# Kernel optimization log

Hardware: AMD Instinct MI355X
Metric: run time of the kernel (lower is better)

Reference implementation:

```python
import jax, jax.numpy as jnp
import numpy as np

N_NODES = 50000
N_EDGES = 1600000
IN_FEATS = 128
ENC_H = 20
DEC_H = 64


def setup_inputs() -> dict:
    key = jax.random.key(0)
    ks = jax.random.split(key, 8)
    x = jax.random.normal(ks[0], (N_NODES, IN_FEATS), dtype=jnp.float32)
    edge_index = jax.random.randint(ks[1], (2, N_EDGES), 0, N_NODES, dtype=jnp.int64)
    eps = jax.random.uniform(ks[2], (N_EDGES, 1), dtype=jnp.float32)
    # GCNConv weight [in, out] and bias
    W_gcn = jax.random.normal(ks[3], (IN_FEATS, ENC_H), dtype=jnp.float32) / np.sqrt(IN_FEATS)
    b_gcn = jnp.zeros((ENC_H,), dtype=jnp.float32)
    # decoder: Linear(60,64) -> ReLU -> Linear(64,1)
    LATENT = 3 * ENC_H
    W1 = jax.random.normal(ks[4], (LATENT, DEC_H), dtype=jnp.float32) / np.sqrt(LATENT)
    b1 = jnp.zeros((DEC_H,), dtype=jnp.float32)
    W2 = jax.random.normal(ks[5], (DEC_H, 1), dtype=jnp.float32) / np.sqrt(DEC_H)
    b2 = jnp.zeros((1,), dtype=jnp.float32)
    return {"x": x, "edge_index": edge_index, "node_id": 123, "eps": eps,
            "W_gcn": W_gcn, "b_gcn": b_gcn, "W1": W1, "b1": b1, "W2": W2, "b2": b2}


def _gcn_conv(x, edge_index, W, b):
    """PyG GCNConv: add self-loops, symmetric norm D^-1/2 (A+I) D^-1/2, x@W + b."""
    N = x.shape[0]
    loop = jnp.arange(N, dtype=edge_index.dtype)
    row = jnp.concatenate([edge_index[0], loop])  # source
    col = jnp.concatenate([edge_index[1], loop])  # target
    deg = jax.ops.segment_sum(jnp.ones_like(col, dtype=x.dtype), col, num_segments=N)
    dinv = jnp.where(deg > 0, jax.lax.rsqrt(deg), 0.0)
    norm = dinv[row] * dinv[col]                 # [E+N]
    h = x @ W                                     # [N, enc_h]
    out = jax.ops.segment_sum(norm[:, None] * h[row], col, num_segments=N)
    return out + b


def reference(x, edge_index, node_id, eps, W_gcn, b_gcn, W1, b1, W2, b2):
    h1 = jax.nn.relu(_gcn_conv(x, edge_index, W_gcn, b_gcn))  # [N, enc_h]
    rows, cols = edge_index[0], edge_index[1]
    E = rows.shape[0]
    node_emb = jnp.broadcast_to(h1[node_id], (E, h1.shape[1]))
    z = jnp.concatenate([h1[rows], h1[cols], node_emb], axis=1)  # [E, 3*enc_h]
    w = jax.nn.relu(z @ W1 + b1) @ W2 + b2                       # [E, 1]
    # gumbel-sigmoid reparameterization (training=True, bias=0.0 -> bias=1e-4)
    bias = 0.0001
    e = (bias - (1.0 - bias)) * eps + (1.0 - bias)
    gate = jnp.log(e) - jnp.log1p(-e) + w  # temperature = 1.0
    return jax.nn.sigmoid(gate)
```

## Files before the change

kernel.cpp:

```cpp
#include <hip/hip_runtime.h>
#include <hip/hip_bf16.h>
#include <math.h>

#define NN 50000
#define NE 1600000
#define FIN 128
#define EH 20
#define DH 64

#define BSTEP 64
#define NBK ((NN + BSTEP - 1) / BSTEP)
#define BCAP 3072
#define CHUNK 8192
#define PERT (CHUNK / 256)


__global__ void k_init(int* bcur, int* off, int* flag, const void* ei) {
    int i = threadIdx.x;
    for (int b = i; b < NBK; b += 1024) bcur[b] = b * BCAP;
    if (i == 0) {
        off[NN] = NE;
        const int* w = (const int*)ei;
        int all0 = 1;
        for (int j = 1; j < 128; j += 2) all0 &= (w[j] == 0);
        *flag = all0;
    }
}

__device__ __forceinline__ int ld_col(const void* ei, int w64, size_t idx) {
    return w64 ? (int)((const long long*)ei)[idx] : ((const int*)ei)[idx];
}

__global__ void k_bin(const void* ei, const int* flag,
                      int* __restrict__ bcur, unsigned* __restrict__ binned) {
    __shared__ int hist[NBK];
    __shared__ int gbase[NBK];
    const int base = blockIdx.x * CHUNK;
    for (int i = threadIdx.x; i < NBK; i += 256) hist[i] = 0;
    __syncthreads();
    const int w64 = *flag;
    int myr[PERT], myc[PERT];
#pragma unroll
    for (int i = 0; i < PERT; ++i) {
        int idx = base + threadIdx.x + i * 256;
        if (idx < NE) {
            myr[i] = ld_col(ei, w64, idx);
            int c = ld_col(ei, w64, (size_t)NE + idx);
            myc[i] = c;
            atomicAdd(&hist[c >> 6], 1);
        } else {
            myc[i] = -1;
        }
    }
    __syncthreads();
    for (int b = threadIdx.x; b < NBK; b += 256) {
        int h = hist[b];
        gbase[b] = h ? atomicAdd(&bcur[b], h) : 0;
        hist[b] = 0;
    }
    __syncthreads();
#pragma unroll
    for (int i = 0; i < PERT; ++i) {
        int c = myc[i];
        if (c >= 0) {
            int bkt = c >> 6;
            int pos = gbase[bkt] + atomicAdd(&hist[bkt], 1);
            binned[pos] = (unsigned)myr[i] | ((unsigned)(c & 63) << 16);
        }
    }
}

__global__ void k_sort(const int* __restrict__ bcur, const unsigned* __restrict__ binned,
                       int* __restrict__ off, int* __restrict__ src) {
    __shared__ int red[256];
    __shared__ int hcnt[BSTEP];
    __shared__ int sc[BSTEP];
    __shared__ int hoff[BSTEP];
    __shared__ int cur[BSTEP];
    const int b = blockIdx.x;
    const int nbase = b * BSTEP;
    int part = 0;
    for (int i = threadIdx.x; i < b; i += 256) part += bcur[i] - i * BCAP;
    red[threadIdx.x] = part;
    __syncthreads();
    for (int d = 128; d > 0; d >>= 1) {
        if (threadIdx.x < d) red[threadIdx.x] += red[threadIdx.x + d];
        __syncthreads();
    }
    const int p0 = red[0];
    const int cnt = bcur[b] - b * BCAP;
    const unsigned* rbase = binned + (size_t)b * BCAP;
    if (threadIdx.x < BSTEP) hcnt[threadIdx.x] = 0;
    __syncthreads();
    for (int i = threadIdx.x; i < cnt; i += 256)
        atomicAdd(&hcnt[rbase[i] >> 16], 1);
    __syncthreads();
    int v = 0;
    if (threadIdx.x < BSTEP) { v = hcnt[threadIdx.x]; sc[threadIdx.x] = v; }
    __syncthreads();
    for (int d = 1; d < BSTEP; d <<= 1) {
        int u = 0;
        if (threadIdx.x < BSTEP && threadIdx.x >= d) u = sc[threadIdx.x - d];
        __syncthreads();
        if (threadIdx.x < BSTEP) sc[threadIdx.x] += u;
        __syncthreads();
    }
    if (threadIdx.x < BSTEP) {
        int o = p0 + sc[threadIdx.x] - v;
        hoff[threadIdx.x] = o;
        cur[threadIdx.x] = 0;
        int n = nbase + threadIdx.x;
        if (n < NN) off[n] = o;
    }
    __syncthreads();
    for (int i = threadIdx.x; i < cnt; i += 256) {
        unsigned rec = rbase[i];
        int cl = rec >> 16;
        int pos = hoff[cl] + atomicAdd(&cur[cl], 1);
        src[pos] = (int)(rec & 0xffffu);
    }
}

__global__ void k_xw(const float* __restrict__ x, const float* __restrict__ W,
                     const int* __restrict__ off, __hip_bfloat16* __restrict__ hs16) {
    int t = blockIdx.x * blockDim.x + threadIdx.x;
    int n = t / EH;
    int k = t - n * EH;
    if (n >= NN) return;
    const float4* xr = (const float4*)(x + (size_t)n * FIN);
    float acc = 0.f;
#pragma unroll
    for (int j4 = 0; j4 < FIN / 4; ++j4) {
        float4 v = xr[j4];
        acc = fmaf(v.x, W[(4 * j4 + 0) * EH + k], acc);
        acc = fmaf(v.y, W[(4 * j4 + 1) * EH + k], acc);
        acc = fmaf(v.z, W[(4 * j4 + 2) * EH + k], acc);
        acc = fmaf(v.w, W[(4 * j4 + 3) * EH + k], acc);
    }
    float dinv = rsqrtf(1.0f + (float)(off[n + 1] - off[n]));
    hs16[n * 32 + k] = __float2bfloat16(dinv * acc);
}

__device__ __forceinline__ float blo(unsigned u) { return __uint_as_float(u << 16); }
__device__ __forceinline__ float bhi(unsigned u) { return __uint_as_float(u & 0xffff0000u); }

__global__ void k_gather(const int* __restrict__ off, const int* __restrict__ src,
                         const __hip_bfloat16* __restrict__ hs16,
                         const float* __restrict__ bg, float* __restrict__ h1) {
    int t = blockIdx.x * blockDim.x + threadIdx.x;
    int n = t / 10;
    int kk = t - n * 10;
    if (n >= NN) return;
    const unsigned* hu = (const unsigned*)hs16;
    unsigned self = hu[n * 16 + kk];
    float acc0 = blo(self), acc1 = bhi(self);
    int e0 = off[n], e1 = off[n + 1];
    int e = e0;
    for (; e + 3 < e1; e += 4) {
        int r0 = src[e];
        int r1 = src[e + 1];
        int r2 = src[e + 2];
        int r3 = src[e + 3];
        unsigned v0 = hu[r0 * 16 + kk];
        unsigned v1 = hu[r1 * 16 + kk];
        unsigned v2 = hu[r2 * 16 + kk];
        unsigned v3 = hu[r3 * 16 + kk];
        acc0 += blo(v0); acc1 += bhi(v0);
        acc0 += blo(v1); acc1 += bhi(v1);
        acc0 += blo(v2); acc1 += bhi(v2);
        acc0 += blo(v3); acc1 += bhi(v3);
    }
    for (; e < e1; ++e) {
        unsigned v = hu[src[e] * 16 + kk];
        acc0 += blo(v); acc1 += bhi(v);
    }
    float dinv = rsqrtf(1.0f + (float)(e1 - e0));
    float2 res;
    res.x = fmaxf(fmaf(dinv, acc0, bg[2 * kk]), 0.f);
    res.y = fmaxf(fmaf(dinv, acc1, bg[2 * kk + 1]), 0.f);
    *(float2*)(h1 + (size_t)n * EH + 2 * kk) = res;
}

__global__ void k_ab(const float* __restrict__ h1, const float* __restrict__ W1,
                     const float* __restrict__ b1, const void* nid_p,
                     __hip_bfloat16* __restrict__ A16, __hip_bfloat16* __restrict__ B16) {
    int t = blockIdx.x * blockDim.x + threadIdx.x;
    int n = t >> 6;
    int j = t & 63;
    if (n >= NN) return;
    int nid = *(const int*)nid_p;
    const float* hr = h1 + (size_t)n * EH;
    const float* hn = h1 + (size_t)nid * EH;
    float a = 0.f, b = b1[j];
#pragma unroll
    for (int k = 0; k < EH; ++k) {
        float hv = hr[k];
        a = fmaf(hv, W1[k * DH + j], a);
        b = fmaf(hv, W1[(EH + k) * DH + j], b);
        b = fmaf(hn[k], W1[(2 * EH + k) * DH + j], b);
    }
    A16[(size_t)n * DH + j] = __float2bfloat16(a);
    B16[(size_t)n * DH + j] = __float2bfloat16(b);
}

__global__ void k_edge(const void* ei, const int* flag,
                       const __hip_bfloat16* __restrict__ A16,
                       const __hip_bfloat16* __restrict__ B16,
                       const float* __restrict__ W2, const float* __restrict__ b2,
                       const float* __restrict__ eps, float* __restrict__ out) {
    long long t = (long long)blockIdx.x * blockDim.x + threadIdx.x;
    int e = (int)(t >> 2);
    if (e >= NE) return;
    int q = (int)(t & 3);
    const int w64 = *flag;
    int r = ld_col(ei, w64, e);
    int c = ld_col(ei, w64, (size_t)NE + e);
    const uint4* arow = (const uint4*)(A16 + (size_t)r * DH) + q * 2;
    const uint4* brow = (const uint4*)(B16 + (size_t)c * DH) + q * 2;
    const float* w = W2 + q * 16;
    float acc = 0.f;
#pragma unroll
    for (int j = 0; j < 2; ++j) {
        uint4 av = arow[j];
        uint4 bv = brow[j];
        acc = fmaf(fmaxf(blo(av.x) + blo(bv.x), 0.f), w[8 * j + 0], acc);
        acc = fmaf(fmaxf(bhi(av.x) + bhi(bv.x), 0.f), w[8 * j + 1], acc);
        acc = fmaf(fmaxf(blo(av.y) + blo(bv.y), 0.f), w[8 * j + 2], acc);
        acc = fmaf(fmaxf(bhi(av.y) + bhi(bv.y), 0.f), w[8 * j + 3], acc);
        acc = fmaf(fmaxf(blo(av.z) + blo(bv.z), 0.f), w[8 * j + 4], acc);
        acc = fmaf(fmaxf(bhi(av.z) + bhi(bv.z), 0.f), w[8 * j + 5], acc);
        acc = fmaf(fmaxf(blo(av.w) + blo(bv.w), 0.f), w[8 * j + 6], acc);
        acc = fmaf(fmaxf(bhi(av.w) + bhi(bv.w), 0.f), w[8 * j + 7], acc);
    }
    acc += __shfl_xor(acc, 1);
    acc += __shfl_xor(acc, 2);
    if (q == 0) {
        float ep = eps[e];
        float ee = fmaf(-0.9998f, ep, 0.9999f);
        float om = fmaf(0.9998f, ep, 0.0001f);
        float gate = 0.69314718f * (__builtin_amdgcn_logf(ee) - __builtin_amdgcn_logf(om))
                   + acc + b2[0];
        float tt = __builtin_amdgcn_exp2f(-1.44269504f * gate);
        out[e] = __builtin_amdgcn_rcpf(1.0f + tt);
    }
}


extern "C" void kernel_launch(void* const* d_in, const int* in_sizes, int n_in,
                              void* d_out, int out_size, void* d_ws, size_t ws_size,
                              hipStream_t stream) {
    const float* x   = (const float*)d_in[0];
    const void*  ei  = d_in[1];
    const void*  nid = d_in[2];
    const float* eps = (const float*)d_in[3];
    const float* Wg  = (const float*)d_in[4];
    const float* bg  = (const float*)d_in[5];
    const float* W1  = (const float*)d_in[6];
    const float* b1  = (const float*)d_in[7];
    const float* W2  = (const float*)d_in[8];
    const float* b2  = (const float*)d_in[9];
    float* out = (float*)d_out;

    float* ws = (float*)d_ws;
    unsigned* binned = (unsigned*)(ws + 0);
    int*  src    = (int*)(ws + 2402560);
    __hip_bfloat16* hs16 = (__hip_bfloat16*)(ws + 4002560);
    float* h1    = ws + 4802560;
    __hip_bfloat16* A16 = (__hip_bfloat16*)(ws + 5802752);
    __hip_bfloat16* B16 = (__hip_bfloat16*)(ws + 7402752);
    int* off     = (int*)(ws + 9002752);
    int* bcur    = (int*)(ws + 9053184);
    int* flag    = (int*)(ws + 9054208);

    dim3 blk(256);
    const int nchunk = (NE + CHUNK - 1) / CHUNK;
    k_init<<<1, 1024, 0, stream>>>(bcur, off, flag, ei);
    k_bin<<<nchunk, blk, 0, stream>>>(ei, flag, bcur, binned);
    k_sort<<<NBK, blk, 0, stream>>>(bcur, binned, off, src);
    k_xw<<<(NN * EH + 255) / 256, blk, 0, stream>>>(x, Wg, off, hs16);
    k_gather<<<(NN * 10 + 255) / 256, blk, 0, stream>>>(off, src, hs16, bg, h1);
    k_ab<<<(NN * 64 + 255) / 256, blk, 0, stream>>>(h1, W1, b1, nid, A16, B16);
    k_edge<<<((size_t)NE * 4 + 255) / 256, blk, 0, stream>>>(ei, flag, A16, B16, W2, b2, eps, out);
}
```

Measured before the change: 174.7 us.

## Process edge MLP in target-bucket order and scatter results back via positions

```diff
diff --git a/kernel.cpp b/kernel.cpp
--- a/kernel.cpp
+++ b/kernel.cpp
@@ -13,6 +13,7 @@
 #define BCAP 3072
 #define CHUNK 8192
 #define PERT (CHUNK / 256)
+#define ESPLIT 4
 
 
 __global__ void k_init(int* bcur, int* off, int* flag, const void* ei) {
@@ -32,7 +33,8 @@
 }
 
 __global__ void k_bin(const void* ei, const int* flag,
-                      int* __restrict__ bcur, unsigned* __restrict__ binned) {
+                      int* __restrict__ bcur, unsigned* __restrict__ binned,
+                      int* __restrict__ pos32) {
     __shared__ int hist[NBK];
     __shared__ int gbase[NBK];
     const int base = blockIdx.x * CHUNK;
@@ -66,6 +68,7 @@
             int bkt = c >> 6;
             int pos = gbase[bkt] + atomicAdd(&hist[bkt], 1);
             binned[pos] = (unsigned)myr[i] | ((unsigned)(c & 63) << 16);
+            pos32[base + threadIdx.x + i * 256] = pos;
         }
     }
 }
@@ -203,46 +206,59 @@
     B16[(size_t)n * DH + j] = __float2bfloat16(b);
 }
 
-__global__ void k_edge(const void* ei, const int* flag,
-                       const __hip_bfloat16* __restrict__ A16,
-                       const __hip_bfloat16* __restrict__ B16,
-                       const float* __restrict__ W2, const float* __restrict__ b2,
-                       const float* __restrict__ eps, float* __restrict__ out) {
-    long long t = (long long)blockIdx.x * blockDim.x + threadIdx.x;
-    int e = (int)(t >> 2);
+__global__ void k_edge_b(const int* __restrict__ bcur,
+                         const unsigned* __restrict__ binned,
+                         const __hip_bfloat16* __restrict__ A16,
+                         const __hip_bfloat16* __restrict__ B16,
+                         const float* __restrict__ W2,
+                         float* __restrict__ stage) {
+    const int b = blockIdx.x / ESPLIT;
+    const int part = blockIdx.x - b * ESPLIT;
+    const int nbase = b * BSTEP;
+    const int cnt = bcur[b] - b * BCAP;
+    const unsigned* rbase = binned + (size_t)b * BCAP;
+    float* sbase = stage + (size_t)b * BCAP;
+    const int q = threadIdx.x & 3;
+    const float* w = W2 + q * 16;
+    for (int i = part * 64 + (threadIdx.x >> 2); i < cnt; i += 64 * ESPLIT) {
+        unsigned rec = rbase[i];
+        int r = (int)(rec & 0xffffu);
+        int cl = (int)(rec >> 16);
+        const uint4* arow = (const uint4*)(A16 + (size_t)r * DH) + q * 2;
+        const uint4* brow = (const uint4*)(B16 + (size_t)(nbase + cl) * DH) + q * 2;
+        float acc = 0.f;
+#pragma unroll
+        for (int j = 0; j < 2; ++j) {
+            uint4 av = arow[j];
+            uint4 bv = brow[j];
+            acc = fmaf(fmaxf(blo(av.x) + blo(bv.x), 0.f), w[8 * j + 0], acc);
+            acc = fmaf(fmaxf(bhi(av.x) + bhi(bv.x), 0.f), w[8 * j + 1], acc);
+            acc = fmaf(fmaxf(blo(av.y) + blo(bv.y), 0.f), w[8 * j + 2], acc);
+            acc = fmaf(fmaxf(bhi(av.y) + bhi(bv.y), 0.f), w[8 * j + 3], acc);
+            acc = fmaf(fmaxf(blo(av.z) + blo(bv.z), 0.f), w[8 * j + 4], acc);
+            acc = fmaf(fmaxf(bhi(av.z) + bhi(bv.z), 0.f), w[8 * j + 5], acc);
+            acc = fmaf(fmaxf(blo(av.w) + blo(bv.w), 0.f), w[8 * j + 6], acc);
+            acc = fmaf(fmaxf(bhi(av.w) + bhi(bv.w), 0.f), w[8 * j + 7], acc);
+        }
+        acc += __shfl_xor(acc, 1);
+        acc += __shfl_xor(acc, 2);
+        if (q == 0) sbase[i] = acc;
+    }
+}
+
+__global__ void k_fin(const int* __restrict__ pos32, const float* __restrict__ stage,
+                      const float* __restrict__ eps, const float* __restrict__ b2,
+                      float* __restrict__ out) {
+    int e = blockIdx.x * blockDim.x + threadIdx.x;
     if (e >= NE) return;
-    int q = (int)(t & 3);
-    const int w64 = *flag;
-    int r = ld_col(ei, w64, e);
-    int c = ld_col(ei, w64, (size_t)NE + e);
-    const uint4* arow = (const uint4*)(A16 + (size_t)r * DH) + q * 2;
-    const uint4* brow = (const uint4*)(B16 + (size_t)c * DH) + q * 2;
-    const float* w = W2 + q * 16;
-    float acc = 0.f;
-#pragma unroll
-    for (int j = 0; j < 2; ++j) {
-        uint4 av = arow[j];
-        uint4 bv = brow[j];
-        acc = fmaf(fmaxf(blo(av.x) + blo(bv.x), 0.f), w[8 * j + 0], acc);
-        acc = fmaf(fmaxf(bhi(av.x) + bhi(bv.x), 0.f), w[8 * j + 1], acc);
-        acc = fmaf(fmaxf(blo(av.y) + blo(bv.y), 0.f), w[8 * j + 2], acc);
-        acc = fmaf(fmaxf(bhi(av.y) + bhi(bv.y), 0.f), w[8 * j + 3], acc);
-        acc = fmaf(fmaxf(blo(av.z) + blo(bv.z), 0.f), w[8 * j + 4], acc);
-        acc = fmaf(fmaxf(bhi(av.z) + bhi(bv.z), 0.f), w[8 * j + 5], acc);
-        acc = fmaf(fmaxf(blo(av.w) + blo(bv.w), 0.f), w[8 * j + 6], acc);
-        acc = fmaf(fmaxf(bhi(av.w) + bhi(bv.w), 0.f), w[8 * j + 7], acc);
-    }
-    acc += __shfl_xor(acc, 1);
-    acc += __shfl_xor(acc, 2);
-    if (q == 0) {
-        float ep = eps[e];
-        float ee = fmaf(-0.9998f, ep, 0.9999f);
-        float om = fmaf(0.9998f, ep, 0.0001f);
-        float gate = 0.69314718f * (__builtin_amdgcn_logf(ee) - __builtin_amdgcn_logf(om))
-                   + acc + b2[0];
-        float tt = __builtin_amdgcn_exp2f(-1.44269504f * gate);
-        out[e] = __builtin_amdgcn_rcpf(1.0f + tt);
-    }
+    float acc = stage[pos32[e]];
+    float ep = eps[e];
+    float ee = fmaf(-0.9998f, ep, 0.9999f);
+    float om = fmaf(0.9998f, ep, 0.0001f);
+    float gate = 0.69314718f * (__builtin_amdgcn_logf(ee) - __builtin_amdgcn_logf(om))
+               + acc + b2[0];
+    float tt = __builtin_amdgcn_exp2f(-1.44269504f * gate);
+    out[e] = __builtin_amdgcn_rcpf(1.0f + tt);
 }
 
 
@@ -264,21 +280,24 @@
     float* ws = (float*)d_ws;
     unsigned* binned = (unsigned*)(ws + 0);
     int*  src    = (int*)(ws + 2402560);
-    __hip_bfloat16* hs16 = (__hip_bfloat16*)(ws + 4002560);
-    float* h1    = ws + 4802560;
-    __hip_bfloat16* A16 = (__hip_bfloat16*)(ws + 5802752);
-    __hip_bfloat16* B16 = (__hip_bfloat16*)(ws + 7402752);
-    int* off     = (int*)(ws + 9002752);
-    int* bcur    = (int*)(ws + 9053184);
-    int* flag    = (int*)(ws + 9054208);
+    int*  pos32  = (int*)(ws + 4002560);
+    __hip_bfloat16* hs16 = (__hip_bfloat16*)(ws + 5602560);
+    float* h1    = ws + 6402560;
+    __hip_bfloat16* A16 = (__hip_bfloat16*)(ws + 7402752);
+    __hip_bfloat16* B16 = (__hip_bfloat16*)(ws + 9002752);
+    float* stage = ws + 10602752;
+    int* off     = (int*)(ws + 13005312);
+    int* bcur    = (int*)(ws + 13055744);
+    int* flag    = (int*)(ws + 13056768);
 
     dim3 blk(256);
     const int nchunk = (NE + CHUNK - 1) / CHUNK;
     k_init<<<1, 1024, 0, stream>>>(bcur, off, flag, ei);
-    k_bin<<<nchunk, blk, 0, stream>>>(ei, flag, bcur, binned);
+    k_bin<<<nchunk, blk, 0, stream>>>(ei, flag, bcur, binned, pos32);
     k_sort<<<NBK, blk, 0, stream>>>(bcur, binned, off, src);
     k_xw<<<(NN * EH + 255) / 256, blk, 0, stream>>>(x, Wg, off, hs16);
     k_gather<<<(NN * 10 + 255) / 256, blk, 0, stream>>>(off, src, hs16, bg, h1);
     k_ab<<<(NN * 64 + 255) / 256, blk, 0, stream>>>(h1, W1, b1, nid, A16, B16);
-    k_edge<<<((size_t)NE * 4 + 255) / 256, blk, 0, stream>>>(ei, flag, A16, B16, W2, b2, eps, out);
-}
+    k_edge_b<<<NBK * ESPLIT, blk, 0, stream>>>(bcur, binned, A16, B16, W2, stage);
+    k_fin<<<(NE + 255) / 256, blk, 0, stream>>>(pos32, stage, eps, b2, out);
+}
```

Measured after the change: 175.5 us. About the same (+0.4%).
